# Kernel tuning notes

Hardware: AMD Instinct MI355X
Metric: run time of the kernel (lower is better)

The kernel has to match this reference:

```python
import jax, jax.numpy as jnp
import numpy as np

RES = 1024
DEPTH = 2.0

def setup_inputs() -> dict:
    key = jax.random.key(0)
    k1, k2 = jax.random.split(key)
    point_cloud = jax.random.normal(k1, (32, 200000, 3), dtype=jnp.float32)
    transformation_matrices = jax.random.normal(k2, (32, 3, 4), dtype=jnp.float32)
    return {"point_cloud": point_cloud, "transformation_matrices": transformation_matrices}

def reference(point_cloud, transformation_matrices):
    B, N, _ = point_cloud.shape
    R = RES
    # homogeneous transform: (B,N,4) @ (B,4,3) -> (B,N,3)
    ones = jnp.ones((B, N, 1), dtype=point_cloud.dtype)
    pc_h = jnp.concatenate([point_cloud, ones], axis=2)
    transformed = jnp.einsum('bnk,bck->bnc', pc_h, transformation_matrices)  # (B,N,3)
    normalized = transformed / DEPTH
    # pixel coords, clamped to [0, R-1]; torch int() truncates (== floor for >=0)
    px = jnp.clip((normalized[:, :, 0] + 1.0) / 2.0 * R, 0.0, R - 1)
    py = jnp.clip((1.0 - normalized[:, :, 1]) / 2.0 * R, 0.0, R - 1)
    xi = jnp.floor(px).astype(jnp.int32)
    yi = jnp.floor(py).astype(jnp.int32)
    z = normalized[:, :, 2]
    b_ids = jnp.arange(B, dtype=jnp.int32)[:, None]
    flat_pix = (b_ids * (R * R) + yi * R + xi).reshape(-1)           # (B*N,)
    gidx = jnp.arange(B * N, dtype=jnp.int32)                        # global point index; within a batch row, larger gidx == larger j
    winners = jax.ops.segment_max(gidx, flat_pix, num_segments=B * R * R)
    valid = winners >= 0                                             # empty segments get int32 min
    safe_w = jnp.clip(winners, 0)
    depth_flat = jnp.where(valid, z.reshape(-1)[safe_w], 0.0)
    depth_map = depth_flat.reshape(B, R, R)
    # F.interpolate to the same (R,R) size with bilinear/align_corners=False is the identity map.
    return depth_map
```

## Files before the change

### kernel.cpp

```cpp
#include <hip/hip_runtime.h>

#define RES   1024
#define NPTS  200000
#define NB    32
#define PPT   16
#define BLK   256
#define NBLK  49
#define BPB   (BLK*PPT)
#define NBAND 256
#define BANDH 4
#define BORD  4096

#define OFF_AR 0
#define OFF_TO 51380224
#define OFF_TC 52985856
#define OFF_BW 54591488

__global__ __launch_bounds__(BLK) void k_bin(
        const float* __restrict__ pc,
        const float* __restrict__ tm,
        unsigned long long* __restrict__ arena,
        unsigned int* __restrict__ toff,
        unsigned int* __restrict__ tcnt,
        int* __restrict__ bwin)
{
#pragma clang fp contract(off)
    const int b   = blockIdx.y;
    const int tid = threadIdx.x;
    const int gg  = b * NBLK + blockIdx.x;

    __shared__ int sb[BORD];
    __shared__ unsigned int hist[NBAND];
    __shared__ unsigned int lofs[NBAND];
    for (int k = tid; k < BORD; k += BLK) sb[k] = -1;
    hist[tid] = 0u;
    __syncthreads();

    const float* M = tm + b * 12;
    const float m0 = M[0], m1 = M[1], m2  = M[2],  m3  = M[3];
    const float m4 = M[4], m5 = M[5], m6  = M[6],  m7  = M[7];
    const float m8 = M[8], m9 = M[9], m10 = M[10], m11 = M[11];

    unsigned long long ent[PPT];
    unsigned int rb[PPT];
    const int base = blockIdx.x * BPB + tid;

    #pragma unroll
    for (int k = 0; k < PPT; ++k) {
        rb[k] = 0xFFFFFFFFu;
        int n = base + k * BLK;
        if (n < NPTS) {
            const float* p = pc + ((size_t)b * NPTS + n) * 3;
            float x = p[0], y = p[1], z = p[2];
            float tx = (x * m0 + y * m1) + (z * m2  + m3);
            float ty = (x * m4 + y * m5) + (z * m6  + m7);
            float tz = (x * m8 + y * m9) + (z * m10 + m11);
            float nx = tx * 0.5f;
            float ny = ty * 0.5f;
            float nz = tz * 0.5f;
            float px = (nx + 1.0f) * 512.0f;
            float py = (1.0f - ny) * 512.0f;
            px = fminf(fmaxf(px, 0.0f), 1023.0f);
            py = fminf(fmaxf(py, 0.0f), 1023.0f);
            int xi = (int)floorf(px);
            int yi = (int)floorf(py);

            bool border = (xi == 0) | (xi == 1023) | (yi == 0) | (yi == 1023);
            if (border) {
                int idx = (yi == 0)    ? xi
                        : (yi == 1023) ? 1024 + xi
                        : (xi == 0)    ? 2048 + yi
                                       : 3072 + yi;
                atomicMax(&sb[idx], n);
            } else {
                int bin = yi >> 2;
                unsigned r = atomicAdd(&hist[bin], 1u);
                rb[k] = ((unsigned)bin << 12) | r;
                unsigned pix = (unsigned)((yi & 3) * RES + xi);
                ent[k] = ((unsigned long long)pix << 52)
                       | ((unsigned long long)(unsigned)n << 32)
                       | (unsigned long long)__float_as_uint(nz);
            }
        }
    }
    __syncthreads();

    if (tid < 64) {
        unsigned carry = 0;
        #pragma unroll
        for (int c = 0; c < 4; ++c) {
            unsigned v = hist[c * 64 + tid];
            unsigned s = v;
            #pragma unroll
            for (int d = 1; d < 64; d <<= 1) {
                unsigned o = __shfl_up(s, d);
                if (tid >= d) s += o;
            }
            lofs[c * 64 + tid] = (s - v) + carry;
            carry += __shfl(s, 63);
        }
    }
    __syncthreads();

    toff[gg * NBAND + tid] = (unsigned)gg * BPB + lofs[tid];
    tcnt[gg * NBAND + tid] = hist[tid];

    #pragma unroll
    for (int k = 0; k < PPT; ++k) {
        if (rb[k] != 0xFFFFFFFFu) {
            unsigned bin = rb[k] >> 12, r = rb[k] & 4095u;
            arena[(size_t)gg * BPB + lofs[bin] + r] = ent[k];
        }
    }

    for (int k = tid; k < BORD; k += BLK) {
        int v = sb[k];
        if (v >= 0) atomicMax(&bwin[b * BORD + k], v);
    }
}

__global__ __launch_bounds__(512) void k_tile(
        const unsigned long long* __restrict__ arena,
        const unsigned int* __restrict__ toff,
        const unsigned int* __restrict__ tcnt,
        const int* __restrict__ bwin,
        const float* __restrict__ pc,
        const float* __restrict__ tm,
        float* __restrict__ out)
{
#pragma clang fp contract(off)
    const int bucket = blockIdx.x;
    const int b = bucket >> 8, band = bucket & 255;
    const int tid = threadIdx.x;

    __shared__ unsigned long long tile[BANDH * RES];
    __shared__ unsigned int stoff[NBLK], scnt[NBLK];
    for (int k = tid; k < BANDH * RES; k += 512) tile[k] = 0ull;
    if (tid < NBLK) {
        stoff[tid] = toff[(b * NBLK + tid) * NBAND + band];
        scnt[tid]  = tcnt[(b * NBLK + tid) * NBAND + band];
    }
    __syncthreads();

    const int wave = tid >> 6, lane = tid & 63;
    for (int g = wave; g < NBLK; g += 8) {
        unsigned off = stoff[g], cnt = scnt[g];
        for (unsigned j = lane; j < cnt; j += 64) {
            unsigned long long e = arena[off + j];
            atomicMax(&tile[e >> 52], e & 0x000FFFFFFFFFFFFFull);
        }
    }
    __syncthreads();

    const float* M2 = tm + b * 12 + 8;
    const float m8 = M2[0], m9 = M2[1], m10 = M2[2], m11 = M2[3];
    const int y0 = band * BANDH;
    const int* bw = bwin + b * BORD;

    for (int r = 0; r < BANDH; ++r) {
        int yi = y0 + r;
        float2 o2;
        #pragma unroll
        for (int h = 0; h < 2; ++h) {
            int xi = tid * 2 + h;
            float zv;
            bool isb = (yi == 0) | (yi == 1023) | (xi == 0) | (xi == 1023);
            if (isb) {
                int n = (yi == 0)    ? bw[xi]
                      : (yi == 1023) ? bw[1024 + xi]
                      : (xi == 0)    ? bw[2048 + yi]
                                     : bw[3072 + yi];
                zv = 0.0f;
                if (n >= 0) {
                    const float* p = pc + ((size_t)b * NPTS + n) * 3;
                    float t = (p[0] * m8 + p[1] * m9) + (p[2] * m10 + m11);
                    zv = t * 0.5f;
                }
            } else {
                zv = __uint_as_float((unsigned)(tile[r * RES + xi] & 0xFFFFFFFFull));
            }
            if (h) o2.y = zv; else o2.x = zv;
        }
        ((float2*)(out + ((size_t)b * RES + yi) * RES))[tid] = o2;
    }
}

extern "C" void kernel_launch(void* const* d_in, const int* in_sizes, int n_in,
                              void* d_out, int out_size, void* d_ws, size_t ws_size,
                              hipStream_t stream)
{
    const float* pc = (const float*)d_in[0];
    const float* tm = (const float*)d_in[1];
    float* out = (float*)d_out;

    char* ws = (char*)d_ws;
    unsigned long long* arena = (unsigned long long*)(ws + OFF_AR);
    unsigned int* toff = (unsigned int*)(ws + OFF_TO);
    unsigned int* tcnt = (unsigned int*)(ws + OFF_TC);
    int*          bwin = (int*)         (ws + OFF_BW);

    hipMemsetAsync(bwin, 0xFF, (size_t)NB * BORD * sizeof(int), stream);

    dim3 g1(NBLK, NB);
    k_bin<<<g1, BLK, 0, stream>>>(pc, tm, arena, toff, tcnt, bwin);

    k_tile<<<NB * NBAND, 512, 0, stream>>>(arena, toff, tcnt, bwin, pc, tm, out);
}
```

Before: 102.7 us.

## Flatten per-bucket gather with prefix-sum search and pack tile metadata

The tile kernel now builds a prefix sum over the 49 per-block counts and lets all 512 threads stride over the combined entry range, using a binary search to find the source segment. Before, each wave walked whole segments, which left lanes idle on short ones. Offset and count are packed into one transposed 32-bit word so each bucket reads contiguous metadata. Two smaller changes go with this: the memset is replaced by a small init kernel, and the output pass reads the shared tile with 128-bit loads. The packing assumes counts and local offsets fit in 16 bits, which holds since each block covers at most 4096 points.

Result: faster. 91.97 us (-10.4%).

```diff
diff --git a/kernel.cpp b/kernel.cpp
--- a/kernel.cpp
+++ b/kernel.cpp
@@ -12,16 +12,20 @@
 #define BORD  4096
 
 #define OFF_AR 0
-#define OFF_TO 51380224
-#define OFF_TC 52985856
-#define OFF_BW 54591488
+#define OFF_TM 51380224
+#define OFF_BW 52985856
+
+__global__ __launch_bounds__(256) void k_init(int4* __restrict__ bwin4)
+{
+    int i = blockIdx.x * 256 + threadIdx.x;
+    bwin4[i] = make_int4(-1, -1, -1, -1);
+}
 
 __global__ __launch_bounds__(BLK) void k_bin(
         const float* __restrict__ pc,
         const float* __restrict__ tm,
         unsigned long long* __restrict__ arena,
-        unsigned int* __restrict__ toff,
-        unsigned int* __restrict__ tcnt,
+        unsigned int* __restrict__ tmeta,
         int* __restrict__ bwin)
 {
 #pragma clang fp contract(off)
@@ -102,8 +106,8 @@
     }
     __syncthreads();
 
-    toff[gg * NBAND + tid] = (unsigned)gg * BPB + lofs[tid];
-    tcnt[gg * NBAND + tid] = hist[tid];
+    tmeta[((size_t)(b * NBAND + tid)) * NBLK + blockIdx.x]
+        = (lofs[tid] << 16) | hist[tid];
 
     #pragma unroll
     for (int k = 0; k < PPT; ++k) {
@@ -121,8 +125,7 @@
 
 __global__ __launch_bounds__(512) void k_tile(
         const unsigned long long* __restrict__ arena,
-        const unsigned int* __restrict__ toff,
-        const unsigned int* __restrict__ tcnt,
+        const unsigned int* __restrict__ tmeta,
         const int* __restrict__ bwin,
         const float* __restrict__ pc,
         const float* __restrict__ tm,
@@ -133,22 +136,41 @@
     const int b = bucket >> 8, band = bucket & 255;
     const int tid = threadIdx.x;
 
-    __shared__ unsigned long long tile[BANDH * RES];
-    __shared__ unsigned int stoff[NBLK], scnt[NBLK];
+    __shared__ __align__(16) unsigned long long tile[BANDH * RES];
+    __shared__ unsigned int pref[NBLK + 1];
+    __shared__ unsigned int sbase[NBLK];
+
     for (int k = tid; k < BANDH * RES; k += 512) tile[k] = 0ull;
-    if (tid < NBLK) {
-        stoff[tid] = toff[(b * NBLK + tid) * NBAND + band];
-        scnt[tid]  = tcnt[(b * NBLK + tid) * NBAND + band];
-    }
-    __syncthreads();
-
-    const int wave = tid >> 6, lane = tid & 63;
-    for (int g = wave; g < NBLK; g += 8) {
-        unsigned off = stoff[g], cnt = scnt[g];
-        for (unsigned j = lane; j < cnt; j += 64) {
-            unsigned long long e = arena[off + j];
-            atomicMax(&tile[e >> 52], e & 0x000FFFFFFFFFFFFFull);
-        }
+
+    unsigned mv = 0;
+    if (tid < NBLK)
+        mv = tmeta[((size_t)(b * NBAND + band)) * NBLK + tid];
+    if (tid < 64) {
+        unsigned cnt = (tid < NBLK) ? (mv & 0xFFFFu) : 0u;
+        unsigned s = cnt;
+        #pragma unroll
+        for (int d = 1; d < 64; d <<= 1) {
+            unsigned o = __shfl_up(s, d);
+            if (tid >= d) s += o;
+        }
+        if (tid < NBLK) {
+            pref[tid + 1] = s;
+            sbase[tid] = (unsigned)((b * NBLK + tid) * BPB) + (mv >> 16);
+        }
+        if (tid == 0) pref[0] = 0u;
+    }
+    __syncthreads();
+
+    const unsigned T = pref[NBLK];
+    for (unsigned idx = tid; idx < T; idx += 512) {
+        int lo = 0, hi = NBLK - 1;
+        #pragma unroll
+        for (int it = 0; it < 6; ++it) {
+            int mid = (lo + hi + 1) >> 1;
+            if (pref[mid] <= idx) lo = mid; else hi = mid - 1;
+        }
+        unsigned long long e = arena[(size_t)sbase[lo] + (idx - pref[lo])];
+        atomicMax(&tile[e >> 52], e & 0x000FFFFFFFFFFFFFull);
     }
     __syncthreads();
 
@@ -159,27 +181,28 @@
 
     for (int r = 0; r < BANDH; ++r) {
         int yi = y0 + r;
+        ulonglong2 kk = ((const ulonglong2*)(tile + r * RES))[tid];
         float2 o2;
+        o2.x = __uint_as_float((unsigned)(kk.x & 0xFFFFFFFFull));
+        o2.y = __uint_as_float((unsigned)(kk.y & 0xFFFFFFFFull));
+
         #pragma unroll
         for (int h = 0; h < 2; ++h) {
             int xi = tid * 2 + h;
-            float zv;
             bool isb = (yi == 0) | (yi == 1023) | (xi == 0) | (xi == 1023);
             if (isb) {
                 int n = (yi == 0)    ? bw[xi]
                       : (yi == 1023) ? bw[1024 + xi]
                       : (xi == 0)    ? bw[2048 + yi]
                                      : bw[3072 + yi];
-                zv = 0.0f;
+                float zv = 0.0f;
                 if (n >= 0) {
                     const float* p = pc + ((size_t)b * NPTS + n) * 3;
                     float t = (p[0] * m8 + p[1] * m9) + (p[2] * m10 + m11);
                     zv = t * 0.5f;
                 }
-            } else {
-                zv = __uint_as_float((unsigned)(tile[r * RES + xi] & 0xFFFFFFFFull));
+                if (h) o2.y = zv; else o2.x = zv;
             }
-            if (h) o2.y = zv; else o2.x = zv;
         }
         ((float2*)(out + ((size_t)b * RES + yi) * RES))[tid] = o2;
     }
@@ -195,14 +218,13 @@
 
     char* ws = (char*)d_ws;
     unsigned long long* arena = (unsigned long long*)(ws + OFF_AR);
-    unsigned int* toff = (unsigned int*)(ws + OFF_TO);
-    unsigned int* tcnt = (unsigned int*)(ws + OFF_TC);
-    int*          bwin = (int*)         (ws + OFF_BW);
-
-    hipMemsetAsync(bwin, 0xFF, (size_t)NB * BORD * sizeof(int), stream);
+    unsigned int* tmeta = (unsigned int*)(ws + OFF_TM);
+    int*          bwin  = (int*)         (ws + OFF_BW);
+
+    k_init<<<(NB * BORD / 4) / 256, 256, 0, stream>>>((int4*)bwin);
 
     dim3 g1(NBLK, NB);
-    k_bin<<<g1, BLK, 0, stream>>>(pc, tm, arena, toff, tcnt, bwin);
-
-    k_tile<<<NB * NBAND, 512, 0, stream>>>(arena, toff, tcnt, bwin, pc, tm, out);
-}
+    k_bin<<<g1, BLK, 0, stream>>>(pc, tm, arena, tmeta, bwin);
+
+    k_tile<<<NB * NBAND, 512, 0, stream>>>(arena, tmeta, bwin, pc, tm, out);
+}
```
